# Optimization experiments

Hardware: AMD Instinct MI355X
Metric: run time of the kernel (lower is better)

## Reference

```python
import jax, jax.numpy as jnp
import numpy as np

B, S, NB, ORDER, D = 256, 50, 8, 2, 128
N_ITEMS, N_RELS = 100000, 200
STDV = 1.0 / float(np.sqrt(D))  # reset_parameters: uniform(-1/sqrt(hidden), 1/sqrt(hidden))


def setup_inputs() -> dict:
    key = jax.random.key(0)
    ks = jax.random.split(key, 24)
    u = lambda k, shape: jax.random.uniform(k, shape, jnp.float32, -STDV, STDV)
    return {
        'h_iids': jax.random.randint(ks[0], (B, S), 1, N_ITEMS),
        'a_iids': jax.random.randint(ks[1], (B,), 0, N_ITEMS),
        'adj_entity': jax.random.randint(ks[2], (N_ITEMS, NB), 0, N_ITEMS),
        'adj_relation': jax.random.randint(ks[3], (N_ITEMS, NB), 0, N_RELS),
        'item_emb': u(ks[4], (N_ITEMS, D)),
        'rel_emb': u(ks[5], (N_RELS, D)),
        'Wa': u(ks[6], (D, 1)), 'ba': u(ks[7], (1,)),          # linear_attention
        'Wt': u(ks[8], (D, D)), 'bt': u(ks[9], (D,)),          # linear_attention_transform
        'Wih': u(ks[10], (D, 3 * D)), 'Whh': u(ks[11], (D, 3 * D)),  # GRU (1 layer)
        'bih': u(ks[12], (3 * D,)), 'bhh': u(ks[13], (3 * D,)),
        'W1': u(ks[14], (D, D)), 'b1': u(ks[15], (D,)),        # linear_one
        'W2': u(ks[16], (D, D)), 'b2': u(ks[17], (D,)),        # linear_two
        'W3': u(ks[18], (D, 1)),                               # linear_three (no bias)
        'Wtr': u(ks[19], (2 * D, D)), 'btr': u(ks[20], (D,)),  # linear_transform
    }


def _forward(h_iids, adj_entity, adj_relation, item_emb, rel_emb,
             Wa, ba, Wt, bt, Wih, Whh, bih, bhh,
             W1, b1, W2, b2, W3, Wtr, btr):
    # ---- get_neighbors: multi-hop KG neighbor expansion ----
    entities = [h_iids]           # level 0: [B, S]
    relations = []
    for i in range(ORDER):
        e = entities[i]
        entities.append(adj_entity[e].reshape(B, -1))    # [B, S*NB^(i+1)]
        relations.append(adj_relation[e].reshape(B, -1))
    ent_embs = [item_emb[e] for e in entities]           # gathers
    rel_embs = [rel_emb[r] for r in relations]
    # ---- high_order_aggregate: attention-weighted neighbor aggregation ----
    neib = ent_embs[ORDER]                                # [B, S*NB^ORDER, D]
    for i in range(ORDER):
        self_e = ent_embs[ORDER - i - 1]                  # [B, M, D]
        rel = rel_embs[ORDER - i - 1].reshape(B, -1, NB, D)
        nb4 = neib.reshape(rel.shape)                     # [B, M, NB, D]
        att = (self_e[:, :, None, :] * rel * nb4) @ Wa + ba   # [B, M, NB, 1]
        alpha = jax.nn.softmax(att, axis=2)
        agg = jnp.sum(nb4 * alpha, axis=2)                # [B, M, D]
        neib = (self_e + agg) @ Wt + bt                   # aggregate='sum' branch
    item_embs = neib                                      # [B, S, D] (sigmoid in src is dead code)
    # ---- GRU, 1 layer, batch_first ----
    def step(h, x):
        gi = x @ Wih + bih
        gh = h @ Whh + bhh
        ir, iz, inn = jnp.split(gi, 3, axis=-1)
        hr, hz, hn = jnp.split(gh, 3, axis=-1)
        r = jax.nn.sigmoid(ir + hr)
        z = jax.nn.sigmoid(iz + hz)
        n = jnp.tanh(inn + r * hn)
        h2 = (1.0 - z) * n + z * h
        return h2, h2
    h0 = jnp.zeros((B, D), jnp.float32)
    _, outs = jax.lax.scan(step, h0, jnp.swapaxes(item_embs, 0, 1))
    output = jnp.swapaxes(outs, 0, 1)                     # [B, S, D]
    # ---- attention pooling over sequence ----
    last_idx = jnp.clip(jnp.sum(h_iids != 0, axis=1) - 1, 0, S - 1)
    local_ht = output[jnp.arange(B), last_idx]            # [B, D]
    q1 = (local_ht @ W1 + b1)[:, None, :]
    q2 = output @ W2 + b2
    al = jax.nn.sigmoid(q1 + q2) @ W3                     # [B, S, 1]
    global_ht = jnp.sum(al * output, axis=1)
    ght = jnp.concatenate([local_ht, global_ht], axis=1) @ Wtr + btr
    logits = jax.nn.relu(ght @ item_emb.T)                # [B, n_items]
    return logits


def reference(h_iids, a_iids, adj_entity, adj_relation, item_emb, rel_emb,
              Wa, ba, Wt, bt, Wih, Whh, bih, bhh,
              W1, b1, W2, b2, W3, Wtr, btr):
    # a_iids is accepted by forward() but unused (matches the torch source).
    return _forward(h_iids, adj_entity, adj_relation, item_emb, rel_emb,
                    Wa, ba, Wt, bt, Wih, Whh, bih, bhh,
                    W1, b1, W2, b2, W3, Wtr, btr)
```

## Files before the change

### kernel.cpp

```cpp
#include <hip/hip_runtime.h>
#include <hip/hip_bf16.h>
#include <math.h>

#define NB_B 256
#define NB_S 50
#define NB_NB 8
#define NB_D 128
#define NB_NITEMS 100000

#define C_RZ (-1.442695041f)
#define C_N (2.885390082f)

typedef __attribute__((ext_vector_type(8))) short short8;
typedef __attribute__((ext_vector_type(4))) float f32x4;
typedef unsigned int uint;
typedef unsigned short ushort;

__device__ __forceinline__ float wave_sum(float t) {
#pragma unroll
  for (int off = 32; off; off >>= 1) t += __shfl_xor(t, off);
  return t;
}

__device__ __forceinline__ ushort f2bf(float f) {
  union { float f; uint u; } v;
  v.f = f;
  return (ushort)((v.u + 0x7fffu + ((v.u >> 16) & 1u)) >> 16);
}
__device__ __forceinline__ uint packbf(float a, float b) {
  return (uint)f2bf(a) | ((uint)f2bf(b) << 16);
}
__device__ __forceinline__ float bflo(uint u) {
  union { uint u; float f; } v; v.u = u << 16; return v.f;
}
__device__ __forceinline__ float bfhi(uint u) {
  union { uint u; float f; } v; v.u = u & 0xffff0000u; return v.f;
}
__device__ __forceinline__ float bf2f(ushort u) {
  union { uint u; float f; } v; v.u = (uint)u << 16; return v.f;
}

__device__ __forceinline__ void castf_body(const float* __restrict__ src,
                                           uint* __restrict__ dst, int i, int n8) {
  if (i >= n8) return;
  float4 a = ((const float4*)src)[2 * i];
  float4 b = ((const float4*)src)[2 * i + 1];
  uint4 o;
  o.x = packbf(a.x, a.y);
  o.y = packbf(a.z, a.w);
  o.z = packbf(b.x, b.y);
  o.w = packbf(b.z, b.w);
  ((uint4*)dst)[i] = o;
}
template <int CO, bool SCALED>
__device__ __forceinline__ void castT_body(const float* __restrict__ W,
                                           ushort* __restrict__ WT, int idx) {
  if (idx >= 128 * CO) return;
  int n = idx >> 7, k = idx & 127;
  float v = W[(size_t)k * CO + n];
  if (SCALED) v *= (n < 256 ? C_RZ : C_N);
  WT[idx] = f2bf(v);
}
__global__ __launch_bounds__(256) void prep_kernel(
    const float* __restrict__ item_emb, const float* __restrict__ rel_emb,
    const float* __restrict__ Wt, const float* __restrict__ Wih,
    const float* __restrict__ Whh, const float* __restrict__ W2,
    const float* __restrict__ bih, const float* __restrict__ bhh,
    uint* __restrict__ EMB_BF, uint* __restrict__ REL_BF,
    ushort* __restrict__ WtT, ushort* __restrict__ WihT,
    ushort* __restrict__ WhhT, ushort* __restrict__ W2T,
    float* __restrict__ GIBIAS) {
  int bx = blockIdx.x, tid = threadIdx.x;
  if (bx < 6250) {
    castf_body(item_emb, EMB_BF, bx * 256 + tid, 1600000);
  } else if (bx < 6263) {
    castf_body(rel_emb, REL_BF, (bx - 6250) * 256 + tid, 3200);
  } else if (bx < 6327) {
    castT_body<128, false>(Wt, WtT, (bx - 6263) * 256 + tid);
  } else if (bx < 6519) {
    castT_body<384, true>(Wih, WihT, (bx - 6327) * 256 + tid);
  } else if (bx < 6711) {
    castT_body<384, true>(Whh, WhhT, (bx - 6519) * 256 + tid);
  } else if (bx < 6775) {
    castT_body<128, false>(W2, W2T, (bx - 6711) * 256 + tid);
  } else {
    int idx = (bx - 6775) * 256 + tid;
    if (idx < 384) {
      float s = (idx < 256) ? C_RZ : C_N;
      GIBIAS[idx] = s * bih[idx] + (idx < 256 ? s * bhh[idx] : 0.f);
    }
  }
}

__device__ __forceinline__ uint hop_pair(
    int e_self, int ln, float wa0, float wa1, const int* __restrict__ adj_e,
    const int* __restrict__ adj_r, const uint* __restrict__ embB,
    const uint* __restrict__ relB, const uint* __restrict__ neibB, int p) {
  uint us = embB[(size_t)e_self * 64 + ln];
  float s0 = bflo(us), s1 = bfhi(us);
  float nb0[NB_NB], nb1[NB_NB], att[NB_NB];
#pragma unroll
  for (int k = 0; k < NB_NB; k++) {
    int r = adj_r[e_self * NB_NB + k];
    uint un;
    if (neibB == nullptr) {
      int e2 = adj_e[e_self * NB_NB + k];
      un = embB[(size_t)e2 * 64 + ln];
    } else {
      un = neibB[((size_t)p * NB_NB + k) * 64 + ln];
    }
    uint ur = relB[r * 64 + ln];
    nb0[k] = bflo(un);
    nb1[k] = bfhi(un);
    float t = s0 * bflo(ur) * nb0[k] * wa0 + s1 * bfhi(ur) * nb1[k] * wa1;
    att[k] = wave_sum(t);
  }
  float den = 0.f, ex[NB_NB];
#pragma unroll
  for (int k = 0; k < NB_NB; k++) { ex[k] = __expf(att[k]); den += ex[k]; }
  float inv = 1.f / den;
  float x0 = s0, x1 = s1;
#pragma unroll
  for (int k = 0; k < NB_NB; k++) {
    float a = ex[k] * inv;
    x0 += a * nb0[k];
    x1 += a * nb1[k];
  }
  return packbf(x0, x1);
}

__global__ __launch_bounds__(256) void hoplin_kernel(
    const int* __restrict__ h_iids, const int* __restrict__ adj_e,
    const int* __restrict__ adj_r, const uint* __restrict__ embB,
    const uint* __restrict__ relB, const float* __restrict__ Wa,
    const ushort* __restrict__ WtT, const float* __restrict__ bt,
    ushort* __restrict__ NEIB) {
  __shared__ ushort X0s[32 * 128];
  const int bx = blockIdx.x;
  const int wv = threadIdx.x >> 6, ln = threadIdx.x & 63;
  float wa0 = Wa[2 * ln], wa1 = Wa[2 * ln + 1];

#pragma unroll
  for (int i = 0; i < 8; i++) {
    int lrow = wv * 8 + i;
    int p = bx * 32 + lrow;
    int b = p / (NB_S * NB_NB);
    int m = p % (NB_S * NB_NB);
    int s = m >> 3, jj = m & 7;
    int h = h_iids[b * NB_S + s];
    int e_self = adj_e[h * NB_NB + jj];
    uint x = hop_pair(e_self, ln, wa0, wa1, adj_e, adj_r, embB, relB, nullptr, p);
    int byte = (lrow * 256 + ln * 4) ^ ((lrow & 7) << 4);
    *(uint*)((char*)X0s + byte) = x;
  }
  __syncthreads();

  const int lr = ln & 15, lg = ln >> 4;
  short8 afr[2][4];
#pragma unroll
  for (int mf = 0; mf < 2; mf++)
#pragma unroll
    for (int kf = 0; kf < 4; kf++) {
      int row = mf * 16 + lr;
      int byte = (row * 256 + lg * 16 + kf * 64) ^ ((row & 7) << 4);
      afr[mf][kf] = *(const short8*)((const char*)X0s + byte);
    }
  f32x4 acc[2][2] = {};
#pragma unroll
  for (int nf = 0; nf < 2; nf++) {
    int n = (wv * 2 + nf) * 16 + lr;
    const ushort* bb = WtT + (size_t)n * 128 + lg * 8;
#pragma unroll
    for (int kf = 0; kf < 4; kf++) {
      short8 b = *(const short8*)(bb + kf * 32);
#pragma unroll
      for (int mf = 0; mf < 2; mf++)
        acc[mf][nf] = __builtin_amdgcn_mfma_f32_16x16x32_bf16(afr[mf][kf], b,
                                                              acc[mf][nf], 0, 0, 0);
    }
  }
#pragma unroll
  for (int mf = 0; mf < 2; mf++)
#pragma unroll
    for (int nf = 0; nf < 2; nf++) {
      int n = (wv * 2 + nf) * 16 + lr;
      float bv = bt[n];
#pragma unroll
      for (int r = 0; r < 4; r++) {
        int mg = bx * 32 + mf * 16 + lg * 4 + r;
        NEIB[(size_t)mg * 128 + n] = f2bf(acc[mf][nf][r] + bv);
      }
    }
}

__global__ __launch_bounds__(256) void hop1_kernel(
    const int* __restrict__ h_iids, const int* __restrict__ adj_e,
    const int* __restrict__ adj_r, const uint* __restrict__ embB,
    const uint* __restrict__ relB, const uint* __restrict__ neibB,
    const float* __restrict__ Wa, uint* __restrict__ Xout, int npairs) {
  int p = (int)((blockIdx.x * blockDim.x + threadIdx.x) >> 6);
  p = __builtin_amdgcn_readfirstlane(p);
  int ln = threadIdx.x & 63;
  if (p >= npairs) return;
  int e_self = h_iids[p];
  float wa0 = Wa[2 * ln], wa1 = Wa[2 * ln + 1];
  Xout[(size_t)p * 64 + ln] =
      hop_pair(e_self, ln, wa0, wa1, adj_e, adj_r, embB, relB, neibB, p);
}

template <int CO, int MPW, bool OUT_BF>
__global__ __launch_bounds__(256) void linm_kernel(
    const ushort* __restrict__ Xbf, const ushort* __restrict__ WT,
    const float* __restrict__ bias, float* __restrict__ Yf,
    ushort* __restrict__ Yb, int nrows) {
  constexpr int NF = CO / 16;
  constexpr int MF = MPW / 16;
  int wave = (int)(blockIdx.x * 4 + (threadIdx.x >> 6));
  int ln = threadIdx.x & 63;
  int m0 = __builtin_amdgcn_readfirstlane(wave) * MPW;
  if (m0 >= nrows) return;
  int lr = ln & 15, lg = ln >> 4;

  short8 afr[MF][4];
#pragma unroll
  for (int mf = 0; mf < MF; mf++) {
    const ushort* ab = Xbf + (size_t)(m0 + mf * 16 + lr) * 128 + lg * 8;
#pragma unroll
    for (int kf = 0; kf < 4; kf++) afr[mf][kf] = *(const short8*)(ab + kf * 32);
  }
  f32x4 acc[MF][NF] = {};
#pragma unroll
  for (int nf = 0; nf < NF; nf++) {
    const ushort* bb = WT + (size_t)(nf * 16 + lr) * 128 + lg * 8;
#pragma unroll
    for (int kf = 0; kf < 4; kf++) {
      short8 b = *(const short8*)(bb + kf * 32);
#pragma unroll
      for (int mf = 0; mf < MF; mf++)
        acc[mf][nf] = __builtin_amdgcn_mfma_f32_16x16x32_bf16(afr[mf][kf], b,
                                                              acc[mf][nf], 0, 0, 0);
    }
  }
#pragma unroll
  for (int mf = 0; mf < MF; mf++)
#pragma unroll
    for (int nf = 0; nf < NF; nf++) {
      int n = nf * 16 + lr;
      float bv = bias[n];
#pragma unroll
      for (int r = 0; r < 4; r++) {
        int m = m0 + mf * 16 + lg * 4 + r;
        float val = acc[mf][nf][r] + bv;
        if (OUT_BF)
          Yb[(size_t)m * CO + n] = f2bf(val);
        else
          Yf[(size_t)m * CO + n] = val;
      }
    }
}

__global__ __launch_bounds__(512) void gru_mfma_kernel(
    const float* __restrict__ GI, const ushort* __restrict__ WhhT_bf,
    const float* __restrict__ bhh, ushort* __restrict__ OUTB) {
  const int b0 = blockIdx.x * 16;
  const int tid = threadIdx.x;
  const int w = tid >> 6, ln = tid & 63;
  const int lr = ln & 15, lg = ln >> 4;
  const int j = w * 16 + lr;

  __shared__ ushort hA[16 * 128];
  __shared__ ushort hB[16 * 128];

  short8 bfr[3][4];
#pragma unroll
  for (int g = 0; g < 3; g++) {
    const ushort* bb = WhhT_bf + (size_t)(g * 128 + j) * 128 + lg * 8;
#pragma unroll
    for (int kf = 0; kf < 4; kf++) bfr[g][kf] = *(const short8*)(bb + kf * 32);
  }
  const float bhn = C_N * bhh[256 + j];

  float h_reg[4] = {0.f, 0.f, 0.f, 0.f};

  {
    uint* hz = (uint*)hA;
#pragma unroll
    for (int i = tid; i < 1024; i += 512) hz[i] = 0;
  }
  __syncthreads();

  float girA[4][3], girB[4][3], girC[4][3], girD[4][3];
#pragma unroll
  for (int r = 0; r < 4; r++) {
    const float* g0 = GI + ((size_t)(b0 + lg * 4 + r) * NB_S + 0) * 384 + j;
    girA[r][0] = g0[0]; girA[r][1] = g0[128]; girA[r][2] = g0[256];
    const float* g1 = GI + ((size_t)(b0 + lg * 4 + r) * NB_S + 1) * 384 + j;
    girB[r][0] = g1[0]; girB[r][1] = g1[128]; girB[r][2] = g1[256];
    const float* g2 = GI + ((size_t)(b0 + lg * 4 + r) * NB_S + 2) * 384 + j;
    girC[r][0] = g2[0]; girC[r][1] = g2[128]; girC[r][2] = g2[256];
  }

  auto STEP = [&](int t, ushort* hRead, ushort* hWrite, float (&cur)[4][3],
                  float (&pre3)[4][3]) {
    if (t + 3 < NB_S) {
#pragma unroll
      for (int r = 0; r < 4; r++) {
        const float* g = GI + ((size_t)(b0 + lg * 4 + r) * NB_S + (t + 3)) * 384 + j;
        pre3[r][0] = g[0]; pre3[r][1] = g[128]; pre3[r][2] = g[256];
      }
    }
    __builtin_amdgcn_sched_barrier(0);
    short8 afr[4];
#pragma unroll
    for (int kf = 0; kf < 4; kf++) {
      int byte = (lr * 256 + kf * 64 + lg * 16) ^ ((lr & 7) << 4);
      afr[kf] = *(const short8*)((const char*)hRead + byte);
    }
    f32x4 acc[3] = {};
#pragma unroll
    for (int g = 0; g < 3; g++)
#pragma unroll
      for (int kf = 0; kf < 4; kf++)
        acc[g] = __builtin_amdgcn_mfma_f32_16x16x32_bf16(afr[kf], bfr[g][kf],
                                                         acc[g], 0, 0, 0);
#pragma unroll
    for (int r = 0; r < 4; r++) {
      int b = lg * 4 + r;
      float rg = __builtin_amdgcn_rcpf(
          1.f + __builtin_amdgcn_exp2f(cur[r][0] + acc[0][r]));
      float ze = __builtin_amdgcn_exp2f(cur[r][1] + acc[1][r]);
      float xp = cur[r][2] + rg * (bhn + acc[2][r]);
      float e2 = __builtin_amdgcn_exp2f(xp);
      float n = 1.f - 2.f * __builtin_amdgcn_rcpf(e2 + 1.f);
      float h2 = n + (h_reg[r] - n) * __builtin_amdgcn_rcpf(1.f + ze);
      h_reg[r] = h2;
      ushort hb = f2bf(h2);
      OUTB[((size_t)(b0 + b) * NB_S + t) * 128 + j] = hb;
      int byte = (b * 256 + j * 2) ^ ((b & 7) << 4);
      *(ushort*)((char*)hWrite + byte) = hb;
    }
    asm volatile("s_waitcnt lgkmcnt(0)" ::: "memory");
    __builtin_amdgcn_s_barrier();
  };

  for (int g4 = 0; g4 < 12; g4++) {
    int t = g4 * 4;
    STEP(t + 0, hA, hB, girA, girD);
    STEP(t + 1, hB, hA, girB, girA);
    STEP(t + 2, hA, hB, girC, girB);
    STEP(t + 3, hB, hA, girD, girC);
  }
  STEP(48, hA, hB, girA, girD);
  STEP(49, hB, hA, girB, girA);
}

__global__ __launch_bounds__(256) void pool_kernel(
    const int* __restrict__ h_iids, const ushort* __restrict__ OUTB,
    const float* __restrict__ W1, const float* __restrict__ b1,
    const ushort* __restrict__ W2T, const float* __restrict__ b2,
    const float* __restrict__ W3, const float* __restrict__ Wtr,
    const float* __restrict__ btr, ushort* __restrict__ GHT_bf) {
  const int b = blockIdx.x, tid = threadIdx.x;
  __shared__ float lh[128];
  __shared__ float q1[128];
  __shared__ float al[64];
  __shared__ float cat[256];

  if (tid < 128) {
    int cnt = 0;
    for (int s = 0; s < NB_S; s++) cnt += (h_iids[b * NB_S + s] != 0);
    int li = min(max(cnt - 1, 0), NB_S - 1);
    lh[tid] = bf2f(OUTB[((size_t)b * NB_S + li) * 128 + tid]);
  }
  __syncthreads();
  if (tid < 128) {
    float acc = b1[tid];
    for (int d = 0; d < 128; d++) acc += lh[d] * W1[(size_t)d * 128 + tid];
    q1[tid] = acc;
  }
  __syncthreads();

  {
    const int wv = tid >> 6, ln = tid & 63, lr = ln & 15, lg = ln >> 4;
    const int s0 = wv * 16;
    short8 zz = {0, 0, 0, 0, 0, 0, 0, 0};
    short8 afr[4];
    int srow = s0 + lr;
#pragma unroll
    for (int kf = 0; kf < 4; kf++)
      afr[kf] = (srow < NB_S)
                    ? *(const short8*)(OUTB + ((size_t)b * NB_S + srow) * 128 +
                                       lg * 8 + kf * 32)
                    : zz;
    float part[4] = {0.f, 0.f, 0.f, 0.f};
#pragma unroll
    for (int nf = 0; nf < 8; nf++) {
      const ushort* bb = W2T + (size_t)(nf * 16 + lr) * 128 + lg * 8;
      f32x4 acc = {};
#pragma unroll
      for (int kf = 0; kf < 4; kf++) {
        short8 bv = *(const short8*)(bb + kf * 32);
        acc = __builtin_amdgcn_mfma_f32_16x16x32_bf16(afr[kf], bv, acc, 0, 0, 0);
      }
      int c = nf * 16 + lr;
      float qc = q1[c] + b2[c];
      float w3 = W3[c];
#pragma unroll
      for (int r = 0; r < 4; r++)
        part[r] += w3 / (1.f + __expf(-(qc + acc[r])));
    }
#pragma unroll
    for (int r = 0; r < 4; r++) {
#pragma unroll
      for (int off = 1; off < 16; off <<= 1) part[r] += __shfl_xor(part[r], off);
      int s = s0 + lg * 4 + r;
      if (lr == 0 && s < NB_S) al[s] = part[r];
    }
  }
  __syncthreads();

  if (tid < 128) {
    float g = 0.f;
    for (int s = 0; s < NB_S; s++)
      g += al[s] * bf2f(OUTB[((size_t)b * NB_S + s) * 128 + tid]);
    cat[tid] = lh[tid];
    cat[128 + tid] = g;
  }
  __syncthreads();
  if (tid < 128) {
    float acc = btr[tid];
    for (int dd = 0; dd < 256; dd++) acc += cat[dd] * Wtr[(size_t)dd * 128 + tid];
    GHT_bf[b * 128 + tid] = f2bf(acc);
  }
}

__global__ __launch_bounds__(256) void logits_mfma_kernel(
    const ushort* __restrict__ GHT_bf, const ushort* __restrict__ embB,
    float* __restrict__ out) {
  int wave = (int)(blockIdx.x * 4 + (threadIdx.x >> 6));
  int ln = threadIdx.x & 63;
  int n0 = __builtin_amdgcn_readfirstlane(wave) * 32;
  if (n0 >= NB_NITEMS) return;
  int lr = ln & 15, lg = ln >> 4;

  short8 bfr[2][4];
#pragma unroll
  for (int nf = 0; nf < 2; nf++) {
    const ushort* base = embB + (size_t)(n0 + nf * 16 + lr) * 128 + lg * 8;
#pragma unroll
    for (int kf = 0; kf < 4; kf++) bfr[nf][kf] = *(const short8*)(base + kf * 32);
  }

  f32x4 acc[16][2] = {};
#pragma unroll
  for (int mg = 0; mg < 4; mg++) {
    short8 afr[4][4];
#pragma unroll
    for (int mf = 0; mf < 4; mf++) {
      const ushort* ab = GHT_bf + (size_t)((mg * 4 + mf) * 16 + lr) * 128 + lg * 8;
#pragma unroll
      for (int kf = 0; kf < 4; kf++) afr[mf][kf] = *(const short8*)(ab + kf * 32);
    }
#pragma unroll
    for (int mf = 0; mf < 4; mf++)
#pragma unroll
      for (int nf = 0; nf < 2; nf++)
#pragma unroll
        for (int kf = 0; kf < 4; kf++)
          acc[mg * 4 + mf][nf] = __builtin_amdgcn_mfma_f32_16x16x32_bf16(
              afr[mf][kf], bfr[nf][kf], acc[mg * 4 + mf][nf], 0, 0, 0);
  }

#pragma unroll
  for (int mf = 0; mf < 16; mf++)
#pragma unroll
    for (int nf = 0; nf < 2; nf++) {
      int n = n0 + nf * 16 + lr;
#pragma unroll
      for (int r = 0; r < 4; r++) {
        int m = mf * 16 + lg * 4 + r;
        out[(size_t)m * NB_NITEMS + n] = fmaxf(acc[mf][nf][r], 0.f);
      }
    }
}

extern "C" void kernel_launch(void* const* d_in, const int* in_sizes, int n_in,
                              void* d_out, int out_size, void* d_ws, size_t ws_size,
                              hipStream_t stream) {
  const int* h_iids = (const int*)d_in[0];
  const int* adj_e = (const int*)d_in[2];
  const int* adj_r = (const int*)d_in[3];
  const float* item_emb = (const float*)d_in[4];
  const float* rel_emb = (const float*)d_in[5];
  const float* Wa = (const float*)d_in[6];
  const float* Wt = (const float*)d_in[8];
  const float* bt = (const float*)d_in[9];
  const float* Wih = (const float*)d_in[10];
  const float* Whh = (const float*)d_in[11];
  const float* bih = (const float*)d_in[12];
  const float* bhh = (const float*)d_in[13];
  const float* W1 = (const float*)d_in[14];
  const float* b1 = (const float*)d_in[15];
  const float* W2 = (const float*)d_in[16];
  const float* b2 = (const float*)d_in[17];
  const float* W3 = (const float*)d_in[18];
  const float* Wtr = (const float*)d_in[19];
  const float* btr = (const float*)d_in[20];
  float* out = (float*)d_out;

  char* w = (char*)d_ws;
  uint* EMB_BF = (uint*)w;                    w += 25600000;
  uint* REL_BF = (uint*)w;                    w += 51200;
  ushort* WtT_bf = (ushort*)w;                w += 32768;
  ushort* WihT_bf = (ushort*)w;               w += 98304;
  ushort* WhhT_bf = (ushort*)w;               w += 98304;
  ushort* W2T_bf = (ushort*)w;                w += 32768;
  float* GIBIAS = (float*)w;                  w += 2048;
  uint* NEIB_bf = (uint*)w;                   w += 26214400;
  uint* X1_bf = (uint*)w;                     w += 3276800;
  uint* SEQ_bf = (uint*)w;                    w += 3276800;
  float* GI = (float*)w;                      w += 19660800;
  ushort* GHT_bf = (ushort*)w;                w += 65536;

  ushort* OUTB = (ushort*)X1_bf;

  prep_kernel<<<6777, 256, 0, stream>>>(item_emb, rel_emb, Wt, Wih, Whh, W2,
                                        bih, bhh, EMB_BF, REL_BF, WtT_bf,
                                        WihT_bf, WhhT_bf, W2T_bf, GIBIAS);

  hoplin_kernel<<<3200, 256, 0, stream>>>(h_iids, adj_e, adj_r, EMB_BF, REL_BF,
                                          Wa, WtT_bf, bt, (ushort*)NEIB_bf);
  hop1_kernel<<<3200, 256, 0, stream>>>(h_iids, adj_e, adj_r, EMB_BF, REL_BF,
                                        NEIB_bf, Wa, X1_bf, 12800);
  linm_kernel<128, 32, true><<<100, 256, 0, stream>>>(
      (const ushort*)X1_bf, WtT_bf, bt, nullptr, (ushort*)SEQ_bf, 12800);
  linm_kernel<384, 16, false><<<200, 256, 0, stream>>>(
      (const ushort*)SEQ_bf, WihT_bf, GIBIAS, GI, nullptr, 12800);

  gru_mfma_kernel<<<16, 512, 0, stream>>>(GI, WhhT_bf, bhh, OUTB);
  pool_kernel<<<256, 256, 0, stream>>>(h_iids, OUTB, W1, b1, W2T_bf, b2, W3,
                                       Wtr, btr, GHT_bf);

  logits_mfma_kernel<<<782, 256, 0, stream>>>(GHT_bf, (const ushort*)EMB_BF, out);
}
```

Measured before the change: 227.7 us.

## Process neighbor aggregation with 16 lanes per pair using 16-byte vector loads

The hop aggregation now assigns 16 lanes per (entity, neighbor-set) pair instead of a full 64-lane wave. Each lane handles 8 dimensions through uint4 loads. The eight attention dot products are reduced together with a transpose-style butterfly of shuffles, which replaces eight full wave reductions. The softmax weights are then shared through LDS. This aims to cut shuffle overhead and raise memory-level parallelism per load, at the cost of more registers per lane. It also relies on an LDS write and read within the same wave with only a waitcnt and no barrier.

```diff
diff --git a/kernel.cpp b/kernel.cpp
--- a/kernel.cpp
+++ b/kernel.cpp
@@ -16,12 +16,6 @@
 typedef unsigned int uint;
 typedef unsigned short ushort;
 
-__device__ __forceinline__ float wave_sum(float t) {
-#pragma unroll
-  for (int off = 32; off; off >>= 1) t += __shfl_xor(t, off);
-  return t;
-}
-
 __device__ __forceinline__ ushort f2bf(float f) {
   union { float f; uint u; } v;
   v.f = f;
@@ -38,6 +32,12 @@
 }
 __device__ __forceinline__ float bf2f(ushort u) {
   union { uint u; float f; } v; v.u = (uint)u << 16; return v.f;
+}
+__device__ __forceinline__ void unpack8(uint4 u, float* f) {
+  f[0] = bflo(u.x); f[1] = bfhi(u.x);
+  f[2] = bflo(u.y); f[3] = bfhi(u.y);
+  f[4] = bflo(u.z); f[5] = bfhi(u.z);
+  f[6] = bflo(u.w); f[7] = bfhi(u.w);
 }
 
 __device__ __forceinline__ void castf_body(const float* __restrict__ src,
@@ -92,41 +92,100 @@
   }
 }
 
-__device__ __forceinline__ uint hop_pair(
-    int e_self, int ln, float wa0, float wa1, const int* __restrict__ adj_e,
+__device__ __forceinline__ uint4 hop_pair4(
+    int e_self, int q, int p, const int* __restrict__ adj_e,
     const int* __restrict__ adj_r, const uint* __restrict__ embB,
-    const uint* __restrict__ relB, const uint* __restrict__ neibB, int p) {
-  uint us = embB[(size_t)e_self * 64 + ln];
-  float s0 = bflo(us), s1 = bfhi(us);
-  float nb0[NB_NB], nb1[NB_NB], att[NB_NB];
-#pragma unroll
-  for (int k = 0; k < NB_NB; k++) {
-    int r = adj_r[e_self * NB_NB + k];
-    uint un;
-    if (neibB == nullptr) {
-      int e2 = adj_e[e_self * NB_NB + k];
-      un = embB[(size_t)e2 * 64 + ln];
-    } else {
-      un = neibB[((size_t)p * NB_NB + k) * 64 + ln];
-    }
-    uint ur = relB[r * 64 + ln];
-    nb0[k] = bflo(un);
-    nb1[k] = bfhi(un);
-    float t = s0 * bflo(ur) * nb0[k] * wa0 + s1 * bfhi(ur) * nb1[k] * wa1;
-    att[k] = wave_sum(t);
-  }
-  float den = 0.f, ex[NB_NB];
-#pragma unroll
-  for (int k = 0; k < NB_NB; k++) { ex[k] = __expf(att[k]); den += ex[k]; }
-  float inv = 1.f / den;
-  float x0 = s0, x1 = s1;
-#pragma unroll
-  for (int k = 0; k < NB_NB; k++) {
-    float a = ex[k] * inv;
-    x0 += a * nb0[k];
-    x1 += a * nb1[k];
-  }
-  return packbf(x0, x1);
+    const uint* __restrict__ relB, const uint* __restrict__ neibB,
+    const float* __restrict__ Wa, float* __restrict__ alds) {
+  uint4 us = ((const uint4*)(embB + (size_t)e_self * 64))[q];
+  float s[8], wa[8], sw[8];
+  unpack8(us, s);
+  *(float4*)&wa[0] = ((const float4*)Wa)[q * 2];
+  *(float4*)&wa[4] = ((const float4*)Wa)[q * 2 + 1];
+#pragma unroll
+  for (int d = 0; d < 8; d++) sw[d] = s[d] * wa[d];
+
+  int4 ra = ((const int4*)(adj_r + (size_t)e_self * 8))[0];
+  int4 rb = ((const int4*)(adj_r + (size_t)e_self * 8))[1];
+  int rk[8] = {ra.x, ra.y, ra.z, ra.w, rb.x, rb.y, rb.z, rb.w};
+
+  uint4 nbp[8];
+  if (neibB == nullptr) {
+    int4 ea = ((const int4*)(adj_e + (size_t)e_self * 8))[0];
+    int4 eb = ((const int4*)(adj_e + (size_t)e_self * 8))[1];
+    int e2[8] = {ea.x, ea.y, ea.z, ea.w, eb.x, eb.y, eb.z, eb.w};
+#pragma unroll
+    for (int k = 0; k < 8; k++)
+      nbp[k] = ((const uint4*)(embB + (size_t)e2[k] * 64))[q];
+  } else {
+#pragma unroll
+    for (int k = 0; k < 8; k++)
+      nbp[k] = ((const uint4*)(neibB + ((size_t)p * 8 + k) * 64))[q];
+  }
+
+  float t[8];
+#pragma unroll
+  for (int k = 0; k < 8; k++) {
+    uint4 ur = ((const uint4*)(relB + (size_t)rk[k] * 64))[q];
+    float rr[8], nb[8];
+    unpack8(ur, rr);
+    unpack8(nbp[k], nb);
+    float tt = 0.f;
+#pragma unroll
+    for (int d = 0; d < 8; d++) tt = fmaf(sw[d] * rr[d], nb[d], tt);
+    t[k] = tt;
+  }
+
+  bool b0 = (q & 1), b1 = (q & 2), b2 = (q & 4);
+  float a4[4];
+#pragma unroll
+  for (int i = 0; i < 4; i++) {
+    float send = b0 ? t[i] : t[4 + i];
+    float recv = __shfl_xor(send, 1);
+    a4[i] = (b0 ? t[4 + i] : t[i]) + recv;
+  }
+  float a2[2];
+#pragma unroll
+  for (int i = 0; i < 2; i++) {
+    float send = b1 ? a4[i] : a4[2 + i];
+    float recv = __shfl_xor(send, 2);
+    a2[i] = (b1 ? a4[2 + i] : a4[i]) + recv;
+  }
+  float send1 = b2 ? a2[0] : a2[1];
+  float recv1 = __shfl_xor(send1, 4);
+  float c = (b2 ? a2[1] : a2[0]) + recv1;
+  c += __shfl_xor(c, 8);
+
+  float e = __expf(c);
+  float den = e;
+  den += __shfl_xor(den, 1);
+  den += __shfl_xor(den, 2);
+  den += __shfl_xor(den, 4);
+  float alpha = e * __builtin_amdgcn_rcpf(den);
+
+  int kstar = (q & 1) * 4 + (q & 2) + ((q & 4) >> 2);
+  if (q < 8) alds[kstar] = alpha;
+  asm volatile("s_waitcnt lgkmcnt(0)" ::: "memory");
+  float a8[8];
+  *(float4*)&a8[0] = ((const float4*)alds)[0];
+  *(float4*)&a8[4] = ((const float4*)alds)[1];
+
+  float x[8];
+#pragma unroll
+  for (int d = 0; d < 8; d++) x[d] = s[d];
+#pragma unroll
+  for (int k = 0; k < 8; k++) {
+    float nb[8];
+    unpack8(nbp[k], nb);
+#pragma unroll
+    for (int d = 0; d < 8; d++) x[d] = fmaf(a8[k], nb[d], x[d]);
+  }
+  uint4 o;
+  o.x = packbf(x[0], x[1]);
+  o.y = packbf(x[2], x[3]);
+  o.z = packbf(x[4], x[5]);
+  o.w = packbf(x[6], x[7]);
+  return o;
 }
 
 __global__ __launch_bounds__(256) void hoplin_kernel(
@@ -136,22 +195,24 @@
     const ushort* __restrict__ WtT, const float* __restrict__ bt,
     ushort* __restrict__ NEIB) {
   __shared__ ushort X0s[32 * 128];
+  __shared__ float als[16][8];
   const int bx = blockIdx.x;
   const int wv = threadIdx.x >> 6, ln = threadIdx.x & 63;
-  float wa0 = Wa[2 * ln], wa1 = Wa[2 * ln + 1];
-
-#pragma unroll
-  for (int i = 0; i < 8; i++) {
-    int lrow = wv * 8 + i;
+  const int g = ln >> 4, q = ln & 15;
+  float* alds = als[wv * 4 + g];
+
+#pragma unroll
+  for (int it = 0; it < 2; it++) {
+    int lrow = wv * 8 + it * 4 + g;
     int p = bx * 32 + lrow;
     int b = p / (NB_S * NB_NB);
     int m = p % (NB_S * NB_NB);
     int s = m >> 3, jj = m & 7;
     int h = h_iids[b * NB_S + s];
     int e_self = adj_e[h * NB_NB + jj];
-    uint x = hop_pair(e_self, ln, wa0, wa1, adj_e, adj_r, embB, relB, nullptr, p);
-    int byte = (lrow * 256 + ln * 4) ^ ((lrow & 7) << 4);
-    *(uint*)((char*)X0s + byte) = x;
+    uint4 o = hop_pair4(e_self, q, p, adj_e, adj_r, embB, relB, nullptr, Wa, alds);
+    int byte = (lrow * 256 + q * 16) ^ ((lrow & 7) << 4);
+    *(uint4*)((char*)X0s + byte) = o;
   }
   __syncthreads();
 
@@ -197,15 +258,15 @@
     const int* __restrict__ h_iids, const int* __restrict__ adj_e,
     const int* __restrict__ adj_r, const uint* __restrict__ embB,
     const uint* __restrict__ relB, const uint* __restrict__ neibB,
-    const float* __restrict__ Wa, uint* __restrict__ Xout, int npairs) {
-  int p = (int)((blockIdx.x * blockDim.x + threadIdx.x) >> 6);
-  p = __builtin_amdgcn_readfirstlane(p);
-  int ln = threadIdx.x & 63;
-  if (p >= npairs) return;
+    const float* __restrict__ Wa, uint* __restrict__ Xout) {
+  __shared__ float als[16][8];
+  const int wv = threadIdx.x >> 6, ln = threadIdx.x & 63;
+  const int g = ln >> 4, q = ln & 15;
+  int p = blockIdx.x * 16 + wv * 4 + g;
   int e_self = h_iids[p];
-  float wa0 = Wa[2 * ln], wa1 = Wa[2 * ln + 1];
-  Xout[(size_t)p * 64 + ln] =
-      hop_pair(e_self, ln, wa0, wa1, adj_e, adj_r, embB, relB, neibB, p);
+  uint4 o = hop_pair4(e_self, q, p, adj_e, adj_r, embB, relB, neibB, Wa,
+                      als[wv * 4 + g]);
+  ((uint4*)(Xout + (size_t)p * 64))[q] = o;
 }
 
 template <int CO, int MPW, bool OUT_BF>
@@ -530,8 +591,8 @@
 
   hoplin_kernel<<<3200, 256, 0, stream>>>(h_iids, adj_e, adj_r, EMB_BF, REL_BF,
                                           Wa, WtT_bf, bt, (ushort*)NEIB_bf);
-  hop1_kernel<<<3200, 256, 0, stream>>>(h_iids, adj_e, adj_r, EMB_BF, REL_BF,
-                                        NEIB_bf, Wa, X1_bf, 12800);
+  hop1_kernel<<<800, 256, 0, stream>>>(h_iids, adj_e, adj_r, EMB_BF, REL_BF,
+                                       NEIB_bf, Wa, X1_bf);
   linm_kernel<128, 32, true><<<100, 256, 0, stream>>>(
       (const ushort*)X1_bf, WtT_bf, bt, nullptr, (ushort*)SEQ_bf, 12800);
   linm_kernel<384, 16, false><<<200, 256, 0, stream>>>(
```

After: 226.9 us. Within noise of the previous version (-0.4%).
